# Performance work log

Hardware: AMD Instinct MI355X
Metric: run time of the kernel (lower is better)

The kernel has to match this reference:

```python
import jax, jax.numpy as jnp
import numpy as np

B, T, C, H = 128, 256, 256, 8
HS = C // H  # 32
EPS = 1e-5


def _layernorm(x, g, b):
    mu = jnp.mean(x, axis=-1, keepdims=True)
    var = jnp.mean(jnp.square(x - mu), axis=-1, keepdims=True)
    return g * (x - mu) / jnp.sqrt(var + EPS) + b


def setup_inputs() -> dict:
    key = jax.random.key(0)
    ks = jax.random.split(key, 12)
    s = 0.02
    return {
        "x": jax.random.normal(ks[0], (B, T, C), dtype=jnp.float32),
        "Wk": jax.random.normal(ks[1], (H, C, HS), dtype=jnp.float32) * s,
        "Wq": jax.random.normal(ks[2], (H, C, HS), dtype=jnp.float32) * s,
        "Wv": jax.random.normal(ks[3], (H, C, HS), dtype=jnp.float32) * s,
        "Wp": jax.random.normal(ks[4], (C, C), dtype=jnp.float32) * s,
        "bp": jnp.zeros((C,), dtype=jnp.float32),
        "W1": jax.random.normal(ks[5], (C, 4 * C), dtype=jnp.float32) * s,
        "b1": jnp.zeros((4 * C,), dtype=jnp.float32),
        "W2": jax.random.normal(ks[6], (4 * C, C), dtype=jnp.float32) * s,
        "b2": jnp.zeros((C,), dtype=jnp.float32),
        "g1": jnp.ones((C,), dtype=jnp.float32),
        "be1": jnp.zeros((C,), dtype=jnp.float32),
        "g2": jnp.ones((C,), dtype=jnp.float32),
        "be2": jnp.zeros((C,), dtype=jnp.float32),
    }


def reference(x, Wk, Wq, Wv, Wp, bp, W1, b1, W2, b2, g1, be1, g2, be2):
    Bx, Tx, Cx = x.shape
    # --- multi-head self-attention on ln1(x) ---
    h = _layernorm(x, g1, be1)
    k = jnp.einsum('btc,hcd->bhtd', h, Wk)
    q = jnp.einsum('btc,hcd->bhtd', h, Wq)
    v = jnp.einsum('btc,hcd->bhtd', h, Wv)
    # NOTE: source computes k @ q^T (transposed vs standard) and scales by C**-0.5
    scores = jnp.einsum('bhtd,bhsd->bhts', k, q) * (Cx ** -0.5)
    mask = jnp.tril(jnp.ones((Tx, Tx), dtype=bool))  # causal lower-triangular
    scores = jnp.where(mask, scores, -jnp.inf)
    w = jax.nn.softmax(scores, axis=-1)
    o = jnp.einsum('bhts,bhsd->bhtd', w, v)
    o = o.transpose(0, 2, 1, 3).reshape(Bx, Tx, Cx)  # concat heads
    x = x + (o @ Wp + bp)
    # --- feed-forward (swish) on ln2(x) ---
    h2 = _layernorm(x, g2, be2)
    f = h2 @ W1 + b1
    f = f * jax.nn.sigmoid(f)  # swish
    f = f @ W2 + b2
    return x + f
```

## Files before the change

kernel.cpp:

```cpp
#include <hip/hip_runtime.h>
#include <cstdint>

#define BB 128
#define TT 256
#define CC 256
#define HH 8
#define HSZ 32
#define NT (BB*TT)
#define CF (4*CC)
#define LN_EPS 1e-5f
#define SCALE 0.0625f

typedef __attribute__((ext_vector_type(8))) __bf16 bf16x8;
typedef __attribute__((ext_vector_type(4))) float f32x4;
typedef __attribute__((ext_vector_type(16))) float f32x16;
typedef __attribute__((ext_vector_type(2))) long i64x2;
typedef unsigned short u16;
typedef unsigned int u32;
typedef unsigned char u8;

__device__ __forceinline__ u16 f2bf(float f) {
  u32 u = __float_as_uint(f);
  u32 r = (u + 0x7fffu + ((u >> 16) & 1u)) >> 16;
  return (u16)r;
}
__device__ __forceinline__ u8 f2f8(float f) {
  return (u8)(__builtin_amdgcn_cvt_pk_fp8_f32(f, f, 0, false) & 0xff);
}
__device__ __forceinline__ u32 f2f8x4(float a, float b, float c, float d) {
  u32 pk = (u32)__builtin_amdgcn_cvt_pk_fp8_f32(a, b, 0, false);
  return (u32)__builtin_amdgcn_cvt_pk_fp8_f32(c, d, (int)pk, true);
}
__device__ __forceinline__ uint2 f2bfx4(float a, float b, float c, float d) {
  uint2 r;
  asm("v_cvt_pk_bf16_f32 %0, %1, %2" : "=v"(r.x) : "v"(a), "v"(b));
  asm("v_cvt_pk_bf16_f32 %0, %1, %2" : "=v"(r.y) : "v"(c), "v"(d));
  return r;
}
__device__ __forceinline__ int swz3i(int r) { return (r ^ (r >> 2)) & 3; }
__device__ __forceinline__ int pkrow(int row, int k) {
  int g = (k >> 4) & 3, h = (k >> 3) & 1, j = k & 7;
  int c = (h << 1) + (g >> 1);
  int cp = c ^ swz3i(row);
  return (k & ~63) + cp * 16 + ((g & 1) << 3) + j;
}

__device__ __forceinline__ void gload16(const void* g, void* l) {
  __builtin_amdgcn_global_load_lds(
      (const __attribute__((address_space(1))) u32*)(uintptr_t)g,
      (__attribute__((address_space(3))) u32*)(u32)(uintptr_t)l,
      16, 0, 0);
}

__device__ __forceinline__ void wait_vm0() {
  asm volatile("s_waitcnt vmcnt(0)" ::: "memory");
  __builtin_amdgcn_sched_barrier(0);
}
__device__ __forceinline__ void wait_vm4() {
  asm volatile("s_waitcnt vmcnt(4)" ::: "memory");
  __builtin_amdgcn_sched_barrier(0);
}
__device__ __forceinline__ void wait_vm8() {
  asm volatile("s_waitcnt vmcnt(8)" ::: "memory");
  __builtin_amdgcn_sched_barrier(0);
}
__device__ __forceinline__ void wait_vm0_lgkm0() {
  asm volatile("s_waitcnt vmcnt(0) lgkmcnt(0)" ::: "memory");
  __builtin_amdgcn_sched_barrier(0);
}
__device__ __forceinline__ void sbar() {
  __builtin_amdgcn_s_barrier();
  __builtin_amdgcn_sched_barrier(0);
}

__global__ __launch_bounds__(256) void conv_ln(
    const float* __restrict__ Wk, const float* __restrict__ Wq,
    const float* __restrict__ Wv, const float* __restrict__ Wp,
    const float* __restrict__ W1, const float* __restrict__ W2,
    u8* __restrict__ WkqvT8, u8* __restrict__ WpT8,
    u8* __restrict__ W1T8, u8* __restrict__ W2T8,
    const float* __restrict__ x, const float* __restrict__ g1,
    const float* __restrict__ be1, u8* __restrict__ hb) {
  __shared__ u8 ldsT[64][68];
  int bid = blockIdx.x, tid = threadIdx.x;
  if (bid >= 192) {
    int wid = tid >> 6, lane = tid & 63;
    int row = (bid - 192) * 4 + wid;
    const float4 v = reinterpret_cast<const float4*>(x + (size_t)row * CC)[lane];
    float s = v.x + v.y + v.z + v.w;
#pragma unroll
    for (int o = 32; o; o >>= 1) s += __shfl_xor(s, o, 64);
    float mu = s * (1.0f / CC);
    float dx = v.x - mu, dy = v.y - mu, dz = v.z - mu, dw = v.w - mu;
    float ss = dx * dx + dy * dy + dz * dz + dw * dw;
#pragma unroll
    for (int o = 32; o; o >>= 1) ss += __shfl_xor(ss, o, 64);
    float inv = rsqrtf(ss * (1.0f / CC) + LN_EPS);
    const float4 gv = reinterpret_cast<const float4*>(g1)[lane];
    const float4 bv = reinterpret_cast<const float4*>(be1)[lane];
    u32 pk = f2f8x4(gv.x * dx * inv + bv.x, gv.y * dy * inv + bv.y,
                    gv.z * dz * inv + bv.z, gv.w * dw * inv + bv.w);
    *reinterpret_cast<u32*>(hb + (size_t)row * CC + pkrow(row, lane * 4)) = pk;
    return;
  }
  int n0, k0, K;
  u8* dst;
  int mode;
  const float* src = nullptr;
  int sk = 0;
  if (bid < 48) {
    mode = 0; n0 = (bid >> 2) * 64; k0 = (bid & 3) * 64; K = 256; dst = WkqvT8;
  } else if (bid < 112) {
    int l = bid - 48;
    mode = 1; n0 = (l >> 2) * 64; k0 = (l & 3) * 64; K = 256; dst = W1T8;
    src = W1; sk = 1024;
  } else if (bid < 176) {
    int l = bid - 112;
    mode = 1; n0 = (l >> 4) * 64; k0 = (l & 15) * 64; K = 1024; dst = W2T8;
    src = W2; sk = 256;
  } else {
    int l = bid - 176;
    mode = 1; n0 = (l >> 2) * 64; k0 = (l & 3) * 64; K = 256; dst = WpT8;
    src = Wp; sk = 256;
  }
  int kr = tid >> 2;
  int nbase = (tid & 3) * 16;
#pragma unroll
  for (int u = 0; u < 4; ++u) {
    int nl = nbase + u * 4;
    int ng = n0 + nl;
    float4 v;
    if (mode == 0) {
      const float* W = (ng < 256) ? Wk : (ng < 512 ? Wq : Wv);
      int inner = ng & 255;
      v = *reinterpret_cast<const float4*>(
          &W[((inner >> 5) << 13) + (size_t)(k0 + kr) * 32 + (inner & 31)]);
    } else {
      v = *reinterpret_cast<const float4*>(
          &src[(size_t)(k0 + kr) * sk + ng]);
    }
    ldsT[nl + 0][kr] = f2f8(v.x);
    ldsT[nl + 1][kr] = f2f8(v.y);
    ldsT[nl + 2][kr] = f2f8(v.z);
    ldsT[nl + 3][kr] = f2f8(v.w);
  }
  __syncthreads();
  int nl = tid >> 2;
  int nglob = n0 + nl;
  int sz = swz3i(nglob);
  u8* drow = dst + (size_t)nglob * K + k0;
#pragma unroll
  for (int c4 = (tid & 3) * 4; c4 < (tid & 3) * 4 + 4; ++c4) {
    int q = c4 >> 1, s = c4 & 1;
    int kb = q * 8 + s * 4;
    u32 pk = (u32)ldsT[nl][kb] | ((u32)ldsT[nl][kb + 1] << 8) |
             ((u32)ldsT[nl][kb + 2] << 16) | ((u32)ldsT[nl][kb + 3] << 24);
    int g = (kb >> 4) & 3, h8 = (kb >> 3) & 1;
    int cp = ((h8 << 1) + (g >> 1)) ^ sz;
    *reinterpret_cast<u32*>(drow + cp * 16 + ((g & 1) << 3) + (kb & 7)) = pk;
  }
}

template <int EPI>
__device__ __forceinline__ void epi_store(f32x4 v, int m, int n,
                                          const float* bias,
                                          const float* resid, void* outp,
                                          int N) {
  size_t off = (size_t)m * N + n;
  if (EPI == 0) {
    u16 pk[4];
#pragma unroll
    for (int r = 0; r < 4; ++r) pk[r] = f2bf(v[r]);
    *reinterpret_cast<uint2*>(&((u16*)outp)[off]) = *reinterpret_cast<uint2*>(pk);
  } else if (EPI == 1) {
    const float4 bv = *reinterpret_cast<const float4*>(&bias[n]);
    const float4 rv = *reinterpret_cast<const float4*>(&resid[off]);
    float4 o;
    o.x = v[0] + bv.x + rv.x;
    o.y = v[1] + bv.y + rv.y;
    o.z = v[2] + bv.z + rv.z;
    o.w = v[3] + bv.w + rv.w;
    *reinterpret_cast<float4*>(&((float*)outp)[off]) = o;
  }
}

template <int NB, int EPI>
__global__ __launch_bounds__(512, 4) void panel_fused(
    const u8* __restrict__ Asrc, const u8* __restrict__ WT8,
    const float* __restrict__ bias, const float* __restrict__ resid,
    void* __restrict__ outp, int N,
    const float* __restrict__ gamma, const float* __restrict__ beta,
    u8* __restrict__ out8) {
  __shared__ u8 Bw[4][256][64];
  __shared__ float red[4][64][2];
  int tid = threadIdx.x;
  int w = tid >> 6, lane = tid & 63;
  int l32 = lane & 31, h = lane >> 5;
  int th = w >> 2, fq = w & 3;
  int m0 = blockIdx.x * 64;

#define STAGEP(nb)                                                            \
  {                                                                           \
    _Pragma("unroll") for (int it = 0; it < 8; ++it) {                        \
      int f = it * 512 + tid;                                                 \
      int kg = f >> 10, t = (f >> 2) & 255, c = f & 3;                        \
      gload16(WT8 + (size_t)((nb) * 256 + t) * 256 + kg * 64 + c * 16,        \
              &Bw[0][0][0] + f * 16);                                         \
    }                                                                         \
  }
  i64x2 aa[4][2];
  {
    int ar = th * 32 + l32;
    int az = swz3i(ar);
#pragma unroll
    for (int kg = 0; kg < 4; ++kg)
#pragma unroll
      for (int p = 0; p < 2; ++p)
        aa[kg][p] = *reinterpret_cast<const i64x2*>(
            Asrc + (size_t)(m0 + ar) * 256 + kg * 64 +
            ((((h << 1) + p) ^ az) << 4));
  }
  STAGEP(0);

#pragma unroll 1
  for (int nb = 0; nb < NB; ++nb) {
    if (nb == 0) wait_vm0(); else wait_vm8();
    sbar();
    f32x16 a1[2] = {};
    __builtin_amdgcn_s_setprio(1);
#pragma unroll
    for (int kg = 0; kg < 4; ++kg) {
#pragma unroll
      for (int p = 0; p < 2; ++p) {
        i64x2 bB[2];
#pragma unroll
        for (int j = 0; j < 2; ++j) {
          int br = fq * 64 + j * 32 + l32, bz = swz3i(br);
          bB[j] = *reinterpret_cast<const i64x2*>(
              &Bw[kg][br][(((h << 1) + p) ^ bz) << 4]);
        }
#pragma unroll
        for (int j = 0; j < 2; ++j) {
          a1[j] = __builtin_amdgcn_mfma_f32_32x32x16_fp8_fp8(
              bB[j][0], aa[kg][p][0], a1[j], 0, 0, 0);
          a1[j] = __builtin_amdgcn_mfma_f32_32x32x16_fp8_fp8(
              bB[j][1], aa[kg][p][1], a1[j], 0, 0, 0);
        }
      }
    }
    __builtin_amdgcn_s_setprio(0);
    sbar();
    if (nb < NB - 1) STAGEP(nb + 1);

    int m = m0 + th * 32 + l32;
    if (EPI == 2) {
      float s1 = 0.f, s2 = 0.f;
#pragma unroll
      for (int j = 0; j < 2; ++j) {
#pragma unroll
        for (int q = 0; q < 4; ++q) {
          int n = fq * 64 + j * 32 + q * 8 + h * 4;
          size_t off = (size_t)m * 256 + n;
          const float4 bv = *reinterpret_cast<const float4*>(&bias[n]);
          const float4 rv = *reinterpret_cast<const float4*>(&resid[off]);
          float4 o;
          o.x = a1[j][q * 4 + 0] + bv.x + rv.x;
          o.y = a1[j][q * 4 + 1] + bv.y + rv.y;
          o.z = a1[j][q * 4 + 2] + bv.z + rv.z;
          o.w = a1[j][q * 4 + 3] + bv.w + rv.w;
          *reinterpret_cast<float4*>(&((float*)outp)[off]) = o;
          a1[j][q * 4 + 0] = o.x; a1[j][q * 4 + 1] = o.y;
          a1[j][q * 4 + 2] = o.z; a1[j][q * 4 + 3] = o.w;
          s1 += (o.x + o.y) + (o.z + o.w);
          s2 += (o.x * o.x + o.y * o.y) + (o.z * o.z + o.w * o.w);
        }
      }
      s1 += __shfl_xor(s1, 32, 64);
      s2 += __shfl_xor(s2, 32, 64);
      if (h == 0) { red[fq][th * 32 + l32][0] = s1; red[fq][th * 32 + l32][1] = s2; }
      sbar();
      int tl = th * 32 + l32;
      float S1 = (red[0][tl][0] + red[1][tl][0]) + (red[2][tl][0] + red[3][tl][0]);
      float S2 = (red[0][tl][1] + red[1][tl][1]) + (red[2][tl][1] + red[3][tl][1]);
      float mu = S1 * (1.0f / 256.0f);
      float inv = rsqrtf(S2 * (1.0f / 256.0f) - mu * mu + LN_EPS);
#pragma unroll
      for (int j = 0; j < 2; ++j) {
#pragma unroll
        for (int q = 0; q < 4; ++q) {
          int n = fq * 64 + j * 32 + q * 8 + h * 4;
          const float4 gv = *reinterpret_cast<const float4*>(&gamma[n]);
          const float4 bb = *reinterpret_cast<const float4*>(&beta[n]);
          u32 pk = f2f8x4(gv.x * (a1[j][q * 4 + 0] - mu) * inv + bb.x,
                          gv.y * (a1[j][q * 4 + 1] - mu) * inv + bb.y,
                          gv.z * (a1[j][q * 4 + 2] - mu) * inv + bb.z,
                          gv.w * (a1[j][q * 4 + 3] - mu) * inv + bb.w);
          *reinterpret_cast<u32*>(out8 + (size_t)m * 256 + pkrow(m, n)) = pk;
        }
      }
    } else {
#pragma unroll
      for (int j = 0; j < 2; ++j) {
#pragma unroll
        for (int q = 0; q < 4; ++q) {
          int n = nb * 256 + fq * 64 + j * 32 + q * 8 + h * 4;
          f32x4 v = {a1[j][q * 4 + 0], a1[j][q * 4 + 1],
                     a1[j][q * 4 + 2], a1[j][q * 4 + 3]};
          epi_store<EPI>(v, m, n, bias, resid, outp, N);
        }
      }
    }
  }
#undef STAGEP
}

__global__ __launch_bounds__(512, 4) void ffn_fused(
    const u8* __restrict__ hb, const u8* __restrict__ W1T8,
    const u8* __restrict__ W2T8, const float* __restrict__ b1,
    const float* __restrict__ b2, const float* __restrict__ x2,
    float* __restrict__ outp) {
  __shared__ u8 Bw1[4][128][64];
  __shared__ u8 Bw2[2][256][64];
  __shared__ u8 Ff[2][64][64];
  __shared__ float b1l[1024];
  int tid = threadIdx.x;
  int w = tid >> 6, lane = tid & 63;
  int l32 = lane & 31, h = lane >> 5;
  int th = w >> 2, fq = w & 3;
  int m0 = blockIdx.x * 64;

#define STAGE_W1(nb)                                                          \
  {                                                                           \
    _Pragma("unroll") for (int it = 0; it < 4; ++it) {                        \
      int f = it * 512 + tid;                                                 \
      int kg = f >> 9, t = (f >> 2) & 127, c = f & 3;                         \
      gload16(W1T8 + (size_t)((nb) * 128 + t) * 256 + kg * 64 + c * 16,       \
              &Bw1[0][0][0] + f * 16);                                        \
    }                                                                         \
  }
#define STAGE_W2(nb)                                                          \
  {                                                                           \
    _Pragma("unroll") for (int it = 0; it < 4; ++it) {                        \
      int f = it * 512 + tid;                                                 \
      int kg2 = f >> 10, o = (f >> 2) & 255, c = f & 3;                       \
      gload16(W2T8 + (size_t)o * 1024 + (nb) * 128 + kg2 * 64 + c * 16,       \
              &Bw2[0][0][0] + f * 16);                                        \
    }                                                                         \
  }
  i64x2 aa[4][2];
  {
    int ar = th * 32 + l32;
    int az = swz3i(ar);
#pragma unroll
    for (int kg = 0; kg < 4; ++kg)
#pragma unroll
      for (int p = 0; p < 2; ++p)
        aa[kg][p] = *reinterpret_cast<const i64x2*>(
            hb + (size_t)(m0 + ar) * 256 + kg * 64 +
            ((((h << 1) + p) ^ az) << 4));
  }
  if (w < 4) gload16(b1 + (size_t)(w * 256 + lane * 4), b1l + w * 256 + lane * 4);
  STAGE_W1(0);
  STAGE_W2(0);

  f32x16 acc2[2] = {};
#pragma unroll 1
  for (int nb = 0; nb < 8; ++nb) {
    wait_vm4();
    sbar();
    f32x16 a1 = {};
    __builtin_amdgcn_s_setprio(1);
#pragma unroll
    for (int kg = 0; kg < 4; ++kg) {
      int br = fq * 32 + l32, bz = swz3i(br);
#pragma unroll
      for (int p = 0; p < 2; ++p) {
        i64x2 bB = *reinterpret_cast<const i64x2*>(
            &Bw1[kg][br][(((h << 1) + p) ^ bz) << 4]);
        a1 = __builtin_amdgcn_mfma_f32_32x32x16_fp8_fp8(
            bB[0], aa[kg][p][0], a1, 0, 0, 0);
        a1 = __builtin_amdgcn_mfma_f32_32x32x16_fp8_fp8(
            bB[1], aa[kg][p][1], a1, 0, 0, 0);
      }
    }
    __builtin_amdgcn_s_setprio(0);
    int kg2w = fq >> 1;
    {
      int t = th * 32 + l32;
      int tz = swz3i(t);
#pragma unroll
      for (int q = 0; q < 4; ++q) {
        int g = (fq & 1) * 2 + (q >> 1);
        int hh = q & 1;
        int c = (hh << 1) + (g >> 1);
        const float4 bv = *reinterpret_cast<const float4*>(
            &b1l[nb * 128 + fq * 32 + q * 8 + h * 4]);
        float bf[4] = {bv.x, bv.y, bv.z, bv.w};
        float sv[4];
#pragma unroll
        for (int r = 0; r < 4; ++r) {
          float fv = a1[q * 4 + r] + bf[r];
          float e = __builtin_amdgcn_exp2f(fv * -1.44269504f);
          sv[r] = fv * __builtin_amdgcn_rcpf(1.0f + e);
        }
        *reinterpret_cast<u32*>(
            &Ff[kg2w][t][((c ^ tz) << 4) + ((g & 1) << 3) + h * 4]) =
            f2f8x4(sv[0], sv[1], sv[2], sv[3]);
      }
    }
    wait_vm0_lgkm0();
    sbar();
    if (nb < 7) STAGE_W1(nb + 1);
    __builtin_amdgcn_s_setprio(1);
#pragma unroll
    for (int kg2 = 0; kg2 < 2; ++kg2)
#pragma unroll
      for (int p = 0; p < 2; ++p) {
        int ar2 = th * 32 + l32;
        i64x2 fa = *reinterpret_cast<const i64x2*>(
            &Ff[kg2][ar2][(((h << 1) + p) ^ swz3i(ar2)) << 4]);
        i64x2 bb2[2];
#pragma unroll
        for (int j = 0; j < 2; ++j) {
          int br = fq * 64 + j * 32 + l32;
          bb2[j] = *reinterpret_cast<const i64x2*>(
              &Bw2[kg2][br][(((h << 1) + p) ^ swz3i(br)) << 4]);
        }
#pragma unroll
        for (int j = 0; j < 2; ++j) {
          acc2[j] = __builtin_amdgcn_mfma_f32_32x32x16_fp8_fp8(
              bb2[j][0], fa[0], acc2[j], 0, 0, 0);
          acc2[j] = __builtin_amdgcn_mfma_f32_32x32x16_fp8_fp8(
              bb2[j][1], fa[1], acc2[j], 0, 0, 0);
        }
      }
    __builtin_amdgcn_s_setprio(0);
    sbar();
    if (nb < 7) STAGE_W2(nb + 1);
  }
#undef STAGE_W1
#undef STAGE_W2
  int m = m0 + th * 32 + l32;
#pragma unroll
  for (int j = 0; j < 2; ++j) {
#pragma unroll
    for (int q = 0; q < 4; ++q) {
      int n = fq * 64 + j * 32 + q * 8 + h * 4;
      f32x4 v = {acc2[j][q * 4 + 0], acc2[j][q * 4 + 1],
                 acc2[j][q * 4 + 2], acc2[j][q * 4 + 3]};
      epi_store<1>(v, m, n, b2, x2, outp, CC);
    }
  }
}

__global__ __launch_bounds__(256) void attn_kernel(const u16* __restrict__ kqv,
                                                   u8* __restrict__ o8) {
  __shared__ u16 q_lds[256 * 32];
  __shared__ u16 vT[32 * 256];
  __shared__ u16 pT[4 * 16 * 64];
  int bh = blockIdx.x;
  int b = bh >> 3, h = bh & 7;
  int tid = threadIdx.x, wid = tid >> 6, lane = tid & 63;
  int l16 = lane & 15, lh = lane >> 4;
  const size_t rowbase = (size_t)b * TT * 768;
  {
    int sr = tid >> 2, c = tid & 3;
    for (int s = sr; s < 256; s += 64) {
      uint4 qv = *reinterpret_cast<const uint4*>(
          &kqv[rowbase + (size_t)s * 768 + 256 + h * 32 + c * 8]);
      *reinterpret_cast<uint4*>((char*)q_lds + ((s * 64 + c * 16) ^ ((s & 7) << 4))) = qv;
      u16 tmp[8];
      *reinterpret_cast<uint4*>(tmp) = *reinterpret_cast<const uint4*>(
          &kqv[rowbase + (size_t)s * 768 + 512 + h * 32 + c * 8]);
#pragma unroll
      for (int e = 0; e < 8; ++e) {
        int d = c * 8 + e;
        vT[d * 256 + (((s >> 3) ^ ((d >> 1) & 7)) << 3) + (s & 7)] = tmp[e];
      }
    }
  }
  __syncthreads();
  u16* pw = &pT[wid * 16 * 64];
  const float C1 = 0.09016844f;
  for (int j = 0; j < 4; ++j) {
    int t16 = (j * 4 + wid) * 16;
    bf16x8 kb = *reinterpret_cast<const bf16x8*>(
        &kqv[rowbase + (size_t)(t16 + l16) * 768 + h * 32 + lh * 8]);
    float m2 = -3e38f, lsum = 0.f;
    f32x4 oacc[2] = {};
    for (int st = 0; st <= j; ++st) {
      int s0 = st << 6;
      float v[4][4];
      float pm[4];
#pragma unroll
      for (int sj = 0; sj < 4; ++sj) {
        int srow = s0 + sj * 16 + l16;
        bf16x8 qa = *reinterpret_cast<const bf16x8*>(
            (char*)q_lds + ((srow * 64 + lh * 16) ^ ((srow & 7) << 4)));
        f32x4 z = {0.f, 0.f, 0.f, 0.f};
        f32x4 sc = __builtin_amdgcn_mfma_f32_16x16x32_bf16(qa, kb, z, 0, 0, 0);
#pragma unroll
        for (int r = 0; r < 4; ++r) {
          float val = sc[r];
          if (st == j) {
            if (sj * 16 + lh * 4 + r > wid * 16 + l16) val = -3e38f;
          }
          v[sj][r] = val;
        }
        pm[sj] = fmaxf(fmaxf(v[sj][0], v[sj][1]), fmaxf(v[sj][2], v[sj][3]));
      }
      float mx = fmaxf(fmaxf(pm[0], pm[1]), fmaxf(pm[2], pm[3]));
      mx = fmaxf(mx, __shfl_xor(mx, 16, 64));
      mx = fmaxf(mx, __shfl_xor(mx, 32, 64));
      float mxs = mx * C1;
      if (!__all(mxs <= m2 + 8.0f)) {
        float mn = fmaxf(m2, mxs);
        float alpha = exp2f(m2 - mn);
        m2 = mn;
        lsum *= alpha;
#pragma unroll
        for (int r = 0; r < 4; ++r) {
          float a = __shfl(alpha, (lane & 48) | (lh * 4 + r), 64);
          oacc[0][r] *= a;
          oacc[1][r] *= a;
        }
      }
#pragma unroll
      for (int sj = 0; sj < 4; ++sj) {
        float p0 = exp2f(__builtin_fmaf(v[sj][0], C1, -m2));
        float p1 = exp2f(__builtin_fmaf(v[sj][1], C1, -m2));
        float p2 = exp2f(__builtin_fmaf(v[sj][2], C1, -m2));
        float p3 = exp2f(__builtin_fmaf(v[sj][3], C1, -m2));
        lsum += (p0 + p1) + (p2 + p3);
        uint2 pkv = f2bfx4(p0, p1, p2, p3);
        *reinterpret_cast<uint2*>(
            (char*)pw + ((l16 * 128 + sj * 32 + lh * 8) ^ ((l16 & 7) << 4))) = pkv;
      }
#pragma unroll
      for (int ks = 0; ks < 2; ++ks) {
        bf16x8 pa = *reinterpret_cast<const bf16x8*>(
            (char*)pw + ((l16 * 128 + ks * 64 + lh * 16) ^ ((l16 & 7) << 4)));
#pragma unroll
        for (int nI = 0; nI < 2; ++nI) {
          int d = nI * 16 + l16;
          int sch = ((s0 + ks * 32 + lh * 8) >> 3) ^ ((d >> 1) & 7);
          bf16x8 vb = *reinterpret_cast<const bf16x8*>(&vT[d * 256 + (sch << 3)]);
          oacc[nI] = __builtin_amdgcn_mfma_f32_16x16x32_bf16(pa, vb, oacc[nI], 0, 0, 0);
        }
      }
    }
    lsum += __shfl_xor(lsum, 16, 64);
    lsum += __shfl_xor(lsum, 32, 64);
#pragma unroll
    for (int r = 0; r < 4; ++r) {
      float ls = __shfl(lsum, (lane & 48) | (lh * 4 + r), 64);
      float inv = 1.0f / ls;
      int t = t16 + lh * 4 + r;
      size_t rb = (size_t)(b * TT + t) * CC;
#pragma unroll
      for (int nI = 0; nI < 2; ++nI) {
        int c = h * HSZ + nI * 16 + l16;
        o8[rb + pkrow(t, c)] = f2f8(oacc[nI][r] * inv);
      }
    }
  }
}

extern "C" void kernel_launch(void* const* d_in, const int* in_sizes, int n_in,
                              void* d_out, int out_size, void* d_ws, size_t ws_size,
                              hipStream_t stream) {
  const float* x   = (const float*)d_in[0];
  const float* Wk  = (const float*)d_in[1];
  const float* Wq  = (const float*)d_in[2];
  const float* Wv  = (const float*)d_in[3];
  const float* Wp  = (const float*)d_in[4];
  const float* bp  = (const float*)d_in[5];
  const float* W1  = (const float*)d_in[6];
  const float* b1  = (const float*)d_in[7];
  const float* W2  = (const float*)d_in[8];
  const float* b2  = (const float*)d_in[9];
  const float* g1  = (const float*)d_in[10];
  const float* be1 = (const float*)d_in[11];
  const float* g2  = (const float*)d_in[12];
  const float* be2 = (const float*)d_in[13];

  char* ws = (char*)d_ws;
  u16* kqv = (u16*)(ws + 0);
  u8*  o8  = (u8*)(ws + 50331648);
  float* x2 = (float*)(ws + 67108864);
  u8*  hb  = (u8*)(ws + 100663296);
  char* wb = ws + 117440512;
  u8*  WkqvT8 = (u8*)(wb);
  u8*  WpT8   = (u8*)(wb + 196608);
  u8*  W1T8   = (u8*)(wb + 196608 + 65536);
  u8*  W2T8   = (u8*)(wb + 196608 + 65536 + 262144);

  conv_ln<<<192 + NT / 4, 256, 0, stream>>>(Wk, Wq, Wv, Wp, W1, W2,
                                            WkqvT8, WpT8, W1T8, W2T8,
                                            x, g1, be1, hb);
  panel_fused<3, 0><<<NT / 64, 512, 0, stream>>>(
      hb, WkqvT8, nullptr, nullptr, kqv, 768, nullptr, nullptr, nullptr);
  attn_kernel<<<BB * HH, 256, 0, stream>>>(kqv, o8);
  panel_fused<1, 2><<<NT / 64, 512, 0, stream>>>(
      o8, WpT8, bp, x, x2, 256, g2, be2, hb);
  ffn_fused<<<NT / 64, 512, 0, stream>>>(hb, W1T8, W2T8, b1, b2, x2, (float*)d_out);
}
```

Baseline: 134.2 us.

## Fuse output projection and LayerNorm2 into FFN kernel, keep residual in registers

Merges the Wp projection, bias plus residual add and LayerNorm2 into the FFN kernel, so x2 is no longer written to or read back from global memory and one kernel launch disappears. The post-attention residual stays in accumulator registers and feeds the final output add. LDS is reused through one shared 64KB buffer for the Wp, W1 and W2 tiles. The normalized activations still round-trip through global hb within the same block. The extra live registers (xw) may lower occupancy.

```diff
diff --git a/kernel.cpp b/kernel.cpp
--- a/kernel.cpp
+++ b/kernel.cpp
@@ -161,38 +161,11 @@
   }
 }
 
-template <int EPI>
-__device__ __forceinline__ void epi_store(f32x4 v, int m, int n,
-                                          const float* bias,
-                                          const float* resid, void* outp,
-                                          int N) {
-  size_t off = (size_t)m * N + n;
-  if (EPI == 0) {
-    u16 pk[4];
-#pragma unroll
-    for (int r = 0; r < 4; ++r) pk[r] = f2bf(v[r]);
-    *reinterpret_cast<uint2*>(&((u16*)outp)[off]) = *reinterpret_cast<uint2*>(pk);
-  } else if (EPI == 1) {
-    const float4 bv = *reinterpret_cast<const float4*>(&bias[n]);
-    const float4 rv = *reinterpret_cast<const float4*>(&resid[off]);
-    float4 o;
-    o.x = v[0] + bv.x + rv.x;
-    o.y = v[1] + bv.y + rv.y;
-    o.z = v[2] + bv.z + rv.z;
-    o.w = v[3] + bv.w + rv.w;
-    *reinterpret_cast<float4*>(&((float*)outp)[off]) = o;
-  }
-}
-
-template <int NB, int EPI>
+template <int NB>
 __global__ __launch_bounds__(512, 4) void panel_fused(
     const u8* __restrict__ Asrc, const u8* __restrict__ WT8,
-    const float* __restrict__ bias, const float* __restrict__ resid,
-    void* __restrict__ outp, int N,
-    const float* __restrict__ gamma, const float* __restrict__ beta,
-    u8* __restrict__ out8) {
+    void* __restrict__ outp, int N) {
   __shared__ u8 Bw[4][256][64];
-  __shared__ float red[4][64][2];
   int tid = threadIdx.x;
   int w = tid >> 6, lane = tid & 63;
   int l32 = lane & 31, h = lane >> 5;
@@ -251,117 +224,158 @@
     __builtin_amdgcn_s_setprio(0);
     sbar();
     if (nb < NB - 1) STAGEP(nb + 1);
-
     int m = m0 + th * 32 + l32;
-    if (EPI == 2) {
-      float s1 = 0.f, s2 = 0.f;
-#pragma unroll
-      for (int j = 0; j < 2; ++j) {
-#pragma unroll
-        for (int q = 0; q < 4; ++q) {
-          int n = fq * 64 + j * 32 + q * 8 + h * 4;
-          size_t off = (size_t)m * 256 + n;
-          const float4 bv = *reinterpret_cast<const float4*>(&bias[n]);
-          const float4 rv = *reinterpret_cast<const float4*>(&resid[off]);
-          float4 o;
-          o.x = a1[j][q * 4 + 0] + bv.x + rv.x;
-          o.y = a1[j][q * 4 + 1] + bv.y + rv.y;
-          o.z = a1[j][q * 4 + 2] + bv.z + rv.z;
-          o.w = a1[j][q * 4 + 3] + bv.w + rv.w;
-          *reinterpret_cast<float4*>(&((float*)outp)[off]) = o;
-          a1[j][q * 4 + 0] = o.x; a1[j][q * 4 + 1] = o.y;
-          a1[j][q * 4 + 2] = o.z; a1[j][q * 4 + 3] = o.w;
-          s1 += (o.x + o.y) + (o.z + o.w);
-          s2 += (o.x * o.x + o.y * o.y) + (o.z * o.z + o.w * o.w);
-        }
-      }
-      s1 += __shfl_xor(s1, 32, 64);
-      s2 += __shfl_xor(s2, 32, 64);
-      if (h == 0) { red[fq][th * 32 + l32][0] = s1; red[fq][th * 32 + l32][1] = s2; }
-      sbar();
-      int tl = th * 32 + l32;
-      float S1 = (red[0][tl][0] + red[1][tl][0]) + (red[2][tl][0] + red[3][tl][0]);
-      float S2 = (red[0][tl][1] + red[1][tl][1]) + (red[2][tl][1] + red[3][tl][1]);
-      float mu = S1 * (1.0f / 256.0f);
-      float inv = rsqrtf(S2 * (1.0f / 256.0f) - mu * mu + LN_EPS);
-#pragma unroll
-      for (int j = 0; j < 2; ++j) {
-#pragma unroll
-        for (int q = 0; q < 4; ++q) {
-          int n = fq * 64 + j * 32 + q * 8 + h * 4;
-          const float4 gv = *reinterpret_cast<const float4*>(&gamma[n]);
-          const float4 bb = *reinterpret_cast<const float4*>(&beta[n]);
-          u32 pk = f2f8x4(gv.x * (a1[j][q * 4 + 0] - mu) * inv + bb.x,
-                          gv.y * (a1[j][q * 4 + 1] - mu) * inv + bb.y,
-                          gv.z * (a1[j][q * 4 + 2] - mu) * inv + bb.z,
-                          gv.w * (a1[j][q * 4 + 3] - mu) * inv + bb.w);
-          *reinterpret_cast<u32*>(out8 + (size_t)m * 256 + pkrow(m, n)) = pk;
-        }
-      }
-    } else {
-#pragma unroll
-      for (int j = 0; j < 2; ++j) {
-#pragma unroll
-        for (int q = 0; q < 4; ++q) {
-          int n = nb * 256 + fq * 64 + j * 32 + q * 8 + h * 4;
-          f32x4 v = {a1[j][q * 4 + 0], a1[j][q * 4 + 1],
-                     a1[j][q * 4 + 2], a1[j][q * 4 + 3]};
-          epi_store<EPI>(v, m, n, bias, resid, outp, N);
-        }
+#pragma unroll
+    for (int j = 0; j < 2; ++j) {
+#pragma unroll
+      for (int q = 0; q < 4; ++q) {
+        int n = nb * 256 + fq * 64 + j * 32 + q * 8 + h * 4;
+        size_t off = (size_t)m * N + n;
+        u16 pk[4];
+#pragma unroll
+        for (int r = 0; r < 4; ++r) pk[r] = f2bf(a1[j][q * 4 + r]);
+        *reinterpret_cast<uint2*>(&((u16*)outp)[off]) =
+            *reinterpret_cast<uint2*>(pk);
       }
     }
   }
 #undef STAGEP
 }
 
-__global__ __launch_bounds__(512, 4) void ffn_fused(
-    const u8* __restrict__ hb, const u8* __restrict__ W1T8,
-    const u8* __restrict__ W2T8, const float* __restrict__ b1,
-    const float* __restrict__ b2, const float* __restrict__ x2,
-    float* __restrict__ outp) {
-  __shared__ u8 Bw1[4][128][64];
-  __shared__ u8 Bw2[2][256][64];
+__global__ __launch_bounds__(512, 4) void wp_ffn(
+    const u8* __restrict__ o8, const u8* __restrict__ WpT8,
+    const float* __restrict__ bp, const float* __restrict__ x,
+    const u8* __restrict__ W1T8, const u8* __restrict__ W2T8,
+    const float* __restrict__ b1, const float* __restrict__ b2,
+    const float* __restrict__ g2, const float* __restrict__ be2,
+    u8* __restrict__ hb, float* __restrict__ outp) {
+  __shared__ u8 Bw[65536];
   __shared__ u8 Ff[2][64][64];
   __shared__ float b1l[1024];
+  __shared__ float red[4][64][2];
   int tid = threadIdx.x;
   int w = tid >> 6, lane = tid & 63;
   int l32 = lane & 31, h = lane >> 5;
   int th = w >> 2, fq = w & 3;
   int m0 = blockIdx.x * 64;
-
-#define STAGE_W1(nb)                                                          \
+  int m = m0 + th * 32 + l32;
+  int ar = th * 32 + l32, az = swz3i(ar);
+
+#define STAGE_W1F(nb)                                                         \
   {                                                                           \
     _Pragma("unroll") for (int it = 0; it < 4; ++it) {                        \
       int f = it * 512 + tid;                                                 \
       int kg = f >> 9, t = (f >> 2) & 127, c = f & 3;                         \
       gload16(W1T8 + (size_t)((nb) * 128 + t) * 256 + kg * 64 + c * 16,       \
-              &Bw1[0][0][0] + f * 16);                                        \
+              Bw + f * 16);                                                   \
     }                                                                         \
   }
-#define STAGE_W2(nb)                                                          \
+#define STAGE_W2F(nb)                                                         \
   {                                                                           \
     _Pragma("unroll") for (int it = 0; it < 4; ++it) {                        \
       int f = it * 512 + tid;                                                 \
       int kg2 = f >> 10, o = (f >> 2) & 255, c = f & 3;                       \
       gload16(W2T8 + (size_t)o * 1024 + (nb) * 128 + kg2 * 64 + c * 16,       \
-              &Bw2[0][0][0] + f * 16);                                        \
+              Bw + 32768 + f * 16);                                           \
     }                                                                         \
   }
+
+  i64x2 aw[4][2];
+#pragma unroll
+  for (int kg = 0; kg < 4; ++kg)
+#pragma unroll
+    for (int p = 0; p < 2; ++p)
+      aw[kg][p] = *reinterpret_cast<const i64x2*>(
+          o8 + (size_t)(m0 + ar) * 256 + kg * 64 + ((((h << 1) + p) ^ az) << 4));
+  {
+#pragma unroll
+    for (int it = 0; it < 8; ++it) {
+      int f = it * 512 + tid;
+      int kg = f >> 10, t = (f >> 2) & 255, c = f & 3;
+      gload16(WpT8 + (size_t)t * 256 + kg * 64 + c * 16, Bw + f * 16);
+    }
+  }
+  wait_vm0();
+  sbar();
+  f32x16 xw[2] = {};
+  __builtin_amdgcn_s_setprio(1);
+#pragma unroll
+  for (int kg = 0; kg < 4; ++kg) {
+#pragma unroll
+    for (int p = 0; p < 2; ++p) {
+      i64x2 bB[2];
+#pragma unroll
+      for (int j = 0; j < 2; ++j) {
+        int br = fq * 64 + j * 32 + l32, bz = swz3i(br);
+        bB[j] = *reinterpret_cast<const i64x2*>(
+            &Bw[kg * 16384 + br * 64 + ((((h << 1) + p) ^ bz) << 4)]);
+      }
+#pragma unroll
+      for (int j = 0; j < 2; ++j) {
+        xw[j] = __builtin_amdgcn_mfma_f32_32x32x16_fp8_fp8(
+            bB[j][0], aw[kg][p][0], xw[j], 0, 0, 0);
+        xw[j] = __builtin_amdgcn_mfma_f32_32x32x16_fp8_fp8(
+            bB[j][1], aw[kg][p][1], xw[j], 0, 0, 0);
+      }
+    }
+  }
+  __builtin_amdgcn_s_setprio(0);
+  sbar();
+  STAGE_W1F(0);
+  STAGE_W2F(0);
+  if (w < 4) gload16(b1 + (size_t)(w * 256 + lane * 4), b1l + w * 256 + lane * 4);
+  float s1 = 0.f, s2 = 0.f;
+#pragma unroll
+  for (int j = 0; j < 2; ++j) {
+#pragma unroll
+    for (int q = 0; q < 4; ++q) {
+      int n = fq * 64 + j * 32 + q * 8 + h * 4;
+      size_t off = (size_t)m * 256 + n;
+      const float4 bv = *reinterpret_cast<const float4*>(&bp[n]);
+      const float4 rv = *reinterpret_cast<const float4*>(&x[off]);
+      float o0 = xw[j][q * 4 + 0] + bv.x + rv.x;
+      float o1 = xw[j][q * 4 + 1] + bv.y + rv.y;
+      float o2 = xw[j][q * 4 + 2] + bv.z + rv.z;
+      float o3 = xw[j][q * 4 + 3] + bv.w + rv.w;
+      xw[j][q * 4 + 0] = o0; xw[j][q * 4 + 1] = o1;
+      xw[j][q * 4 + 2] = o2; xw[j][q * 4 + 3] = o3;
+      s1 += (o0 + o1) + (o2 + o3);
+      s2 += (o0 * o0 + o1 * o1) + (o2 * o2 + o3 * o3);
+    }
+  }
+  s1 += __shfl_xor(s1, 32, 64);
+  s2 += __shfl_xor(s2, 32, 64);
+  if (h == 0) { red[fq][ar][0] = s1; red[fq][ar][1] = s2; }
+  sbar();
+  {
+    float S1 = (red[0][ar][0] + red[1][ar][0]) + (red[2][ar][0] + red[3][ar][0]);
+    float S2 = (red[0][ar][1] + red[1][ar][1]) + (red[2][ar][1] + red[3][ar][1]);
+    float mu = S1 * (1.0f / 256.0f);
+    float inv = rsqrtf(S2 * (1.0f / 256.0f) - mu * mu + LN_EPS);
+#pragma unroll
+    for (int j = 0; j < 2; ++j) {
+#pragma unroll
+      for (int q = 0; q < 4; ++q) {
+        int n = fq * 64 + j * 32 + q * 8 + h * 4;
+        const float4 gv = *reinterpret_cast<const float4*>(&g2[n]);
+        const float4 bb = *reinterpret_cast<const float4*>(&be2[n]);
+        u32 pk = f2f8x4(gv.x * (xw[j][q * 4 + 0] - mu) * inv + bb.x,
+                        gv.y * (xw[j][q * 4 + 1] - mu) * inv + bb.y,
+                        gv.z * (xw[j][q * 4 + 2] - mu) * inv + bb.z,
+                        gv.w * (xw[j][q * 4 + 3] - mu) * inv + bb.w);
+        *reinterpret_cast<u32*>(hb + (size_t)m * 256 + pkrow(m, n)) = pk;
+      }
+    }
+  }
+  wait_vm0();
+  sbar();
   i64x2 aa[4][2];
-  {
-    int ar = th * 32 + l32;
-    int az = swz3i(ar);
-#pragma unroll
-    for (int kg = 0; kg < 4; ++kg)
-#pragma unroll
-      for (int p = 0; p < 2; ++p)
-        aa[kg][p] = *reinterpret_cast<const i64x2*>(
-            hb + (size_t)(m0 + ar) * 256 + kg * 64 +
-            ((((h << 1) + p) ^ az) << 4));
-  }
-  if (w < 4) gload16(b1 + (size_t)(w * 256 + lane * 4), b1l + w * 256 + lane * 4);
-  STAGE_W1(0);
-  STAGE_W2(0);
+#pragma unroll
+  for (int kg = 0; kg < 4; ++kg)
+#pragma unroll
+    for (int p = 0; p < 2; ++p)
+      aa[kg][p] = *reinterpret_cast<const i64x2*>(
+          hb + (size_t)(m0 + ar) * 256 + kg * 64 + ((((h << 1) + p) ^ az) << 4));
 
   f32x16 acc2[2] = {};
 #pragma unroll 1
@@ -376,7 +390,7 @@
 #pragma unroll
       for (int p = 0; p < 2; ++p) {
         i64x2 bB = *reinterpret_cast<const i64x2*>(
-            &Bw1[kg][br][(((h << 1) + p) ^ bz) << 4]);
+            &Bw[kg * 8192 + br * 64 + ((((h << 1) + p) ^ bz) << 4)]);
         a1 = __builtin_amdgcn_mfma_f32_32x32x16_fp8_fp8(
             bB[0], aa[kg][p][0], a1, 0, 0, 0);
         a1 = __builtin_amdgcn_mfma_f32_32x32x16_fp8_fp8(
@@ -386,8 +400,7 @@
     __builtin_amdgcn_s_setprio(0);
     int kg2w = fq >> 1;
     {
-      int t = th * 32 + l32;
-      int tz = swz3i(t);
+      int tz = swz3i(ar);
 #pragma unroll
       for (int q = 0; q < 4; ++q) {
         int g = (fq & 1) * 2 + (q >> 1);
@@ -404,27 +417,27 @@
           sv[r] = fv * __builtin_amdgcn_rcpf(1.0f + e);
         }
         *reinterpret_cast<u32*>(
-            &Ff[kg2w][t][((c ^ tz) << 4) + ((g & 1) << 3) + h * 4]) =
+            &Ff[kg2w][ar][((c ^ tz) << 4) + ((g & 1) << 3) + h * 4]) =
             f2f8x4(sv[0], sv[1], sv[2], sv[3]);
       }
     }
     wait_vm0_lgkm0();
     sbar();
-    if (nb < 7) STAGE_W1(nb + 1);
+    if (nb < 7) STAGE_W1F(nb + 1);
     __builtin_amdgcn_s_setprio(1);
 #pragma unroll
     for (int kg2 = 0; kg2 < 2; ++kg2)
 #pragma unroll
       for (int p = 0; p < 2; ++p) {
-        int ar2 = th * 32 + l32;
         i64x2 fa = *reinterpret_cast<const i64x2*>(
-            &Ff[kg2][ar2][(((h << 1) + p) ^ swz3i(ar2)) << 4]);
+            &Ff[kg2][ar][(((h << 1) + p) ^ swz3i(ar)) << 4]);
         i64x2 bb2[2];
 #pragma unroll
         for (int j = 0; j < 2; ++j) {
           int br = fq * 64 + j * 32 + l32;
           bb2[j] = *reinterpret_cast<const i64x2*>(
-              &Bw2[kg2][br][(((h << 1) + p) ^ swz3i(br)) << 4]);
+              &Bw[32768 + kg2 * 16384 + br * 64 +
+                  ((((h << 1) + p) ^ swz3i(br)) << 4)]);
         }
 #pragma unroll
         for (int j = 0; j < 2; ++j) {
@@ -436,19 +449,23 @@
       }
     __builtin_amdgcn_s_setprio(0);
     sbar();
-    if (nb < 7) STAGE_W2(nb + 1);
-  }
-#undef STAGE_W1
-#undef STAGE_W2
-  int m = m0 + th * 32 + l32;
+    if (nb < 7) STAGE_W2F(nb + 1);
+  }
+#undef STAGE_W1F
+#undef STAGE_W2F
 #pragma unroll
   for (int j = 0; j < 2; ++j) {
 #pragma unroll
     for (int q = 0; q < 4; ++q) {
       int n = fq * 64 + j * 32 + q * 8 + h * 4;
-      f32x4 v = {acc2[j][q * 4 + 0], acc2[j][q * 4 + 1],
-                 acc2[j][q * 4 + 2], acc2[j][q * 4 + 3]};
-      epi_store<1>(v, m, n, b2, x2, outp, CC);
+      size_t off = (size_t)m * 256 + n;
+      const float4 bv = *reinterpret_cast<const float4*>(&b2[n]);
+      float4 o;
+      o.x = acc2[j][q * 4 + 0] + bv.x + xw[j][q * 4 + 0];
+      o.y = acc2[j][q * 4 + 1] + bv.y + xw[j][q * 4 + 1];
+      o.z = acc2[j][q * 4 + 2] + bv.z + xw[j][q * 4 + 2];
+      o.w = acc2[j][q * 4 + 3] + bv.w + xw[j][q * 4 + 3];
+      *reinterpret_cast<float4*>(&outp[off]) = o;
     }
   }
 }
@@ -587,7 +604,6 @@
   char* ws = (char*)d_ws;
   u16* kqv = (u16*)(ws + 0);
   u8*  o8  = (u8*)(ws + 50331648);
-  float* x2 = (float*)(ws + 67108864);
   u8*  hb  = (u8*)(ws + 100663296);
   char* wb = ws + 117440512;
   u8*  WkqvT8 = (u8*)(wb);
@@ -598,10 +614,8 @@
   conv_ln<<<192 + NT / 4, 256, 0, stream>>>(Wk, Wq, Wv, Wp, W1, W2,
                                             WkqvT8, WpT8, W1T8, W2T8,
                                             x, g1, be1, hb);
-  panel_fused<3, 0><<<NT / 64, 512, 0, stream>>>(
-      hb, WkqvT8, nullptr, nullptr, kqv, 768, nullptr, nullptr, nullptr);
+  panel_fused<3><<<NT / 64, 512, 0, stream>>>(hb, WkqvT8, kqv, 768);
   attn_kernel<<<BB * HH, 256, 0, stream>>>(kqv, o8);
-  panel_fused<1, 2><<<NT / 64, 512, 0, stream>>>(
-      o8, WpT8, bp, x, x2, 256, g2, be2, hb);
-  ffn_fused<<<NT / 64, 512, 0, stream>>>(hb, W1T8, W2T8, b1, b2, x2, (float*)d_out);
-}
+  wp_ffn<<<NT / 64, 512, 0, stream>>>(o8, WpT8, bp, x, W1T8, W2T8,
+                                      b1, b2, g2, be2, hb, (float*)d_out);
+}
```

Result: faster. 126.1 us (-6.0%).
